# Kernel optimization log

Measured on AMD Instinct MI355X. Metric: run time of the kernel, lower is better.

Reference implementation:

```python
import jax, jax.numpy as jnp
import numpy as np

RADIUS = 0.2
NSAMPLE = 32
BANDWIDTH = 0.1


def ellipsoid_query(xyz, new_xyz, radius, nsample):
    """xyz:(B,N,3), new_xyz:(B,P,3) -> idx:(B,P,nsample) int32.
    Ellipsoid semi-axes (radius, 2*radius, radius); first nsample hits,
    padded with the first hit (index 0 if empty), matching the CUDA kernel.
    """
    B, N, _ = xyz.shape
    inv_sq = jnp.asarray([1.0 / radius**2, 1.0 / (2.0 * radius) ** 2, 1.0 / radius**2],
                         dtype=xyz.dtype)
    # accumulate per-coordinate to avoid a (B,P,N,3) intermediate
    q = jnp.zeros((B, new_xyz.shape[1], N), dtype=xyz.dtype)
    for k in range(3):
        d = new_xyz[:, :, None, k] - xyz[:, None, :, k]  # (B,P,N)
        q = q + d * d * inv_sq[k]
    mask = q < 1.0
    cand = jnp.where(mask, jnp.arange(N, dtype=jnp.int32), jnp.int32(N))  # invalid -> N
    cand = jnp.sort(cand, axis=-1)[..., :nsample]                          # (B,P,S)
    first = cand[..., :1]
    first = jnp.where(first >= N, jnp.int32(0), first)
    return jnp.where(cand >= N, first, cand)


def group(features, idx):
    """features:(B,C,N), idx:(B,P,S) -> (B,C,P,S)"""
    return jnp.take_along_axis(features[:, :, None, :], idx[:, None, :, :], axis=-1)


def setup_inputs() -> dict:
    key = jax.random.key(0)
    k1, k2, k3 = jax.random.split(key, 3)
    xyz = jax.random.uniform(k1, (4, 8192, 3), dtype=jnp.float32)
    new_xyz = jax.random.uniform(k2, (4, 2048, 3), dtype=jnp.float32)
    features = jax.random.normal(k3, (4, 64, 8192), dtype=jnp.float32)
    return {"xyz": xyz, "new_xyz": new_xyz, "features": features}


def reference(xyz, new_xyz, features):
    idx = ellipsoid_query(xyz, new_xyz, RADIUS, NSAMPLE)          # (B,P,S)
    xyz_trans = jnp.transpose(xyz, (0, 2, 1))                      # (B,3,N)
    grouped_xyz = group(xyz_trans, idx)                            # (B,3,P,S)
    # density: gaussian of distance to center
    g = jnp.transpose(grouped_xyz, (0, 2, 3, 1))                   # (B,P,S,3)
    dist = jnp.linalg.norm(g - new_xyz[:, :, None, :], axis=-1)    # (B,P,S)
    density = jnp.exp(-dist**2 / (2.0 * BANDWIDTH**2)) / (2.5 * BANDWIDTH)
    grouped_density = (1.0 / density)[:, None, :, :]               # (B,1,P,S)
    grouped_features = group(features, idx)                        # (B,C,P,S)
    return jnp.concatenate([grouped_xyz, grouped_density, grouped_features], axis=1)
```

## Files before the change

kernel.cpp:

```cpp
#include <hip/hip_runtime.h>

constexpr int NPTS = 8192;
constexpr int NQ   = 2048;
constexpr int NC   = 64;
constexpr int NS   = 32;
constexpr int NCH  = 3 + 1 + NC;
constexpr int CS   = NQ * NS;
constexpr int TP   = 2048;
constexpr int QPB  = 8;



union KLds {
    struct {
        float pts[3][TP + 1];
        int   idx[QPB][NS];
        int   ndone;
    } s;
    float tile[NC][65];
};

__device__ __forceinline__ unsigned prefix_popc(unsigned long long m) {
    return __builtin_amdgcn_mbcnt_hi((unsigned)(m >> 32),
           __builtin_amdgcn_mbcnt_lo((unsigned)m, 0u));
}

__global__ __launch_bounds__(512, 8) void scan_trans_kernel(
    const float* __restrict__ xyz,
    const float* __restrict__ nxyz,
    const float* __restrict__ feat,
    float* __restrict__ ftr,
    int* __restrict__ gidx,
    float* __restrict__ out,
    int ntrans)
{
    __shared__ KLds u;
    const int bx = blockIdx.x;
    const int t  = threadIdx.x;

    if (bx < ntrans) {
        const int b  = bx >> 7;
        const int tl = bx & 127;
        const int n0 = tl * 64;
        const float* fb = feat + (size_t)b * NC * NPTS;
        const int pl = t & 63;
        const int c0 = t >> 6;
        #pragma unroll
        for (int i = 0; i < 8; ++i) {
            const int c = c0 + 8 * i;
            u.tile[c][pl] = fb[(size_t)c * NPTS + n0 + pl];
        }
        __syncthreads();
        float* tb = ftr + ((size_t)b * NPTS + n0) * NC;
        #pragma unroll
        for (int i = 0; i < 8; ++i) {
            const int pp = c0 + 8 * i;
            tb[(size_t)pp * NC + pl] = u.tile[pl][pp];
        }
        return;
    }

    const int sb   = bx - ntrans;
    const int qpb  = NQ / QPB;
    const int b    = sb / qpb;
    const int p0   = (sb - b * qpb) * QPB;
    const int lane = t & 63;
    const int wave = t >> 6;
    const int p    = p0 + wave;
    const float* xb = xyz + (size_t)b * NPTS * 3;
    int* idx_row = u.s.idx[wave];

    const float qx = nxyz[((size_t)b * NQ + p) * 3 + 0];
    const float qy = nxyz[((size_t)b * NQ + p) * 3 + 1];
    const float qz = nxyz[((size_t)b * NQ + p) * 3 + 2];

    int cnt = 0;
    int first = -1;
    if (t == 0) u.s.ndone = 0;

    for (int tb = 0; tb < NPTS / TP; ++tb) {
        const float* src = xb + (size_t)tb * TP * 3;
        #pragma unroll
        for (int k = 0; k < 3 * TP / 512; ++k) {
            const int g  = k * 512 + t;
            const float val = src[g];
            const int pt = g / 3;
            const int c  = g - 3 * pt;
            u.s.pts[c][pt] = val;
        }
        __syncthreads();

        if (cnt < NS) {
            const int boff = tb * TP;
            for (int base = 0; base < TP; base += 128) {
                const int i0 = base + lane;
                const int i1 = i0 + 64;
                const float xA = u.s.pts[0][i0], xB = u.s.pts[0][i1];
                const float yA = u.s.pts[1][i0], yB = u.s.pts[1][i1];
                const float zA = u.s.pts[2][i0], zB = u.s.pts[2][i1];

                const float dxA = __fsub_rn(qx, xA);
                const float dyA = __fsub_rn(qy, yA);
                const float dzA = __fsub_rn(qz, zA);
                const float qA  = __fadd_rn(__fadd_rn(
                                    __fmul_rn(__fmul_rn(dxA, dxA), 25.0f),
                                    __fmul_rn(__fmul_rn(dyA, dyA), 6.25f)),
                                    __fmul_rn(__fmul_rn(dzA, dzA), 25.0f));
                const float dxB = __fsub_rn(qx, xB);
                const float dyB = __fsub_rn(qy, yB);
                const float dzB = __fsub_rn(qz, zB);
                const float qB  = __fadd_rn(__fadd_rn(
                                    __fmul_rn(__fmul_rn(dxB, dxB), 25.0f),
                                    __fmul_rn(__fmul_rn(dyB, dyB), 6.25f)),
                                    __fmul_rn(__fmul_rn(dzB, dzB), 25.0f));
                const bool hitA = qA < 1.0f;
                const bool hitB = qB < 1.0f;

                const unsigned long long m0 = __ballot(hitA);
                const unsigned long long m1 = __ballot(hitB);
                if (first < 0) {
                    if (m0 != 0ull)      first = boff + base + __builtin_ctzll(m0);
                    else if (m1 != 0ull) first = boff + base + 64 + __builtin_ctzll(m1);
                }
                if (hitA) {
                    const int pos = cnt + (int)prefix_popc(m0);
                    if (pos < NS) idx_row[pos] = boff + i0;
                }
                const int c0h = __popcll(m0);
                if (hitB) {
                    const int pos = cnt + c0h + (int)prefix_popc(m1);
                    if (pos < NS) idx_row[pos] = boff + i1;
                }
                cnt += c0h + __popcll(m1);
                if (cnt >= NS) break;
            }
            if (cnt >= NS && lane == 0)
                atomicAdd(&u.s.ndone, 1);
        }
        __syncthreads();
        if (u.s.ndone == QPB) break;
    }

    if (cnt < NS) {
        const int f = (cnt == 0) ? 0 : first;
        if (lane < NS && lane >= cnt) idx_row[lane] = f;
    }

    if (lane < NS) {
        const int s = lane;
        const int j = idx_row[s];
        gidx[((size_t)b * NQ + p) * NS + s] = j;

        const float px = xb[3 * j + 0];
        const float py = xb[3 * j + 1];
        const float pz = xb[3 * j + 2];
        const float dx = __fsub_rn(px, qx);
        const float dy = __fsub_rn(py, qy);
        const float dz = __fsub_rn(pz, qz);
        const float d2 = __fadd_rn(__fadd_rn(__fmul_rn(dx, dx), __fmul_rn(dy, dy)),
                                   __fmul_rn(dz, dz));
        const float dist = __fsqrt_rn(d2);
        const float arg  = __fdiv_rn(-__fmul_rn(dist, dist), 0.02f);
        const float density = __fmul_rn(expf(arg), 4.0f);
        const float gd = __fdiv_rn(1.0f, density);

        float* ob = out + ((size_t)b * NCH * NQ + p) * NS + s;
        ob[0 * (size_t)CS] = px;
        ob[1 * (size_t)CS] = py;
        ob[2 * (size_t)CS] = pz;
        ob[3 * (size_t)CS] = gd;
    }
}

__global__ __launch_bounds__(512, 8) void group_kernel(
    const int* __restrict__ gidx,
    const float* __restrict__ ftr,
    float* __restrict__ out,
    int B)
{
    __shared__ float ldsc[NC][33];

    const int g = blockIdx.x;
    int b, p;
    if (B == 4) {
        b = (g & 7) >> 1;
        p = ((g >> 3) << 1) | (g & 1);
    } else {
        b = g / NQ;
        p = g - b * NQ;
    }
    const int tid = threadIdx.x;

    const int cg = tid & 15;
    const int sl = tid >> 4;
    const int j  = gidx[((size_t)b * NQ + p) * NS + sl];
    const float4 v = ((const float4*)(ftr + ((size_t)b * NPTS + j) * NC))[cg];
    ldsc[4 * cg + 0][sl] = v.x;
    ldsc[4 * cg + 1][sl] = v.y;
    ldsc[4 * cg + 2][sl] = v.z;
    ldsc[4 * cg + 3][sl] = v.w;
    __syncthreads();

    const int c  = tid >> 3;
    const int s4 = (tid & 7) << 2;
    float4 w;
    w.x = ldsc[c][s4 + 0];
    w.y = ldsc[c][s4 + 1];
    w.z = ldsc[c][s4 + 2];
    w.w = ldsc[c][s4 + 3];
    float* op = out + (((size_t)b * NCH + 4 + c) * NQ + p) * NS + s4;
    *(float4*)op = w;
}

__global__ __launch_bounds__(512, 8) void ellip_direct_kernel(
    const float* __restrict__ xyz,
    const float* __restrict__ nxyz,
    const float* __restrict__ feat,
    float* __restrict__ out)
{
    __shared__ int idx_s[8][NS];

    const int b    = blockIdx.y;
    const int p0   = blockIdx.x * 8;
    const int tid  = threadIdx.x;
    const int lane = tid & 63;
    const int wave = tid >> 6;
    const float* xb = xyz + (size_t)b * NPTS * 3;

    {
        const int p = p0 + wave;
        const float qx = nxyz[((size_t)b * NQ + p) * 3 + 0];
        const float qy = nxyz[((size_t)b * NQ + p) * 3 + 1];
        const float qz = nxyz[((size_t)b * NQ + p) * 3 + 2];
        int cnt = 0, first = -1;
        for (int base = 0; base < NPTS; base += 64) {
            const int i = base + lane;
            const float dx = __fsub_rn(qx, xb[i * 3 + 0]);
            const float dy = __fsub_rn(qy, xb[i * 3 + 1]);
            const float dz = __fsub_rn(qz, xb[i * 3 + 2]);
            const float t0 = __fmul_rn(__fmul_rn(dx, dx), 25.0f);
            const float t1 = __fmul_rn(__fmul_rn(dy, dy), 6.25f);
            const float t2 = __fmul_rn(__fmul_rn(dz, dz), 25.0f);
            const float qv = __fadd_rn(__fadd_rn(t0, t1), t2);
            const bool hit = qv < 1.0f;
            const unsigned long long m = __ballot(hit);
            if (first < 0 && m != 0ull) first = base + __builtin_ctzll(m);
            if (hit) {
                const int pos = cnt + __popcll(m & ((1ull << lane) - 1ull));
                if (pos < NS) idx_s[wave][pos] = i;
            }
            cnt += __popcll(m);
            if (cnt >= NS) break;
        }
        if (cnt < NS) {
            const int f = (cnt == 0) ? 0 : first;
            if (lane < NS && lane >= cnt) idx_s[wave][lane] = f;
        }
    }
    __syncthreads();

    const int s = tid & 31;
    const int h = (tid >> 5) & 1;
    const int q = tid >> 6;
    const int p = p0 + q;
    const int j = idx_s[q][s];
    float* ob = out + ((size_t)b * NCH * NQ + p) * NS + s;

    if (h == 0) {
        const float qx = nxyz[((size_t)b * NQ + p) * 3 + 0];
        const float qy = nxyz[((size_t)b * NQ + p) * 3 + 1];
        const float qz = nxyz[((size_t)b * NQ + p) * 3 + 2];
        const float px = xb[j * 3 + 0], py = xb[j * 3 + 1], pz = xb[j * 3 + 2];
        const float dx = __fsub_rn(px, qx);
        const float dy = __fsub_rn(py, qy);
        const float dz = __fsub_rn(pz, qz);
        const float d2 = __fadd_rn(__fadd_rn(__fmul_rn(dx, dx), __fmul_rn(dy, dy)),
                                   __fmul_rn(dz, dz));
        const float dist = __fsqrt_rn(d2);
        const float arg  = __fdiv_rn(-__fmul_rn(dist, dist), 0.02f);
        const float gd = __fdiv_rn(1.0f, __fmul_rn(expf(arg), 4.0f));
        ob[0 * (size_t)CS] = px;
        ob[1 * (size_t)CS] = py;
        ob[2 * (size_t)CS] = pz;
        ob[3 * (size_t)CS] = gd;
    }
    const float* fb = feat + (size_t)b * NC * NPTS + j;
    #pragma unroll 4
    for (int c = h; c < NC; c += 2)
        ob[(size_t)(4 + c) * CS] = fb[(size_t)c * NPTS];
}

extern "C" void kernel_launch(void* const* d_in, const int* in_sizes, int n_in,
                              void* d_out, int out_size, void* d_ws, size_t ws_size,
                              hipStream_t stream) {
    const float* xyz  = (const float*)d_in[0];
    const float* nxyz = (const float*)d_in[1];
    const float* feat = (const float*)d_in[2];
    float* out = (float*)d_out;

    const int B = in_sizes[0] / (NPTS * 3);
    const size_t ftr_f = (size_t)B * NPTS * NC;
    const size_t idx_f = (size_t)B * NQ * NS;
    const size_t need  = (ftr_f + idx_f) * 4;

    if (ws_size >= need) {
        float* ftr = (float*)d_ws;
        int*   idx = (int*)(ftr + ftr_f);

        const int ntrans = B * (NPTS / 64);
        const int nscan  = B * (NQ / QPB);
        scan_trans_kernel<<<dim3(ntrans + nscan), 512, 0, stream>>>(
            xyz, nxyz, feat, ftr, idx, out, ntrans);
        group_kernel<<<dim3(B * NQ), 512, 0, stream>>>(idx, ftr, out, B);
    } else {
        ellip_direct_kernel<<<dim3(NQ / 8, B), 512, 0, stream>>>(xyz, nxyz, feat, out);
    }
}
```

Measured before the change: 101.0 us.

## Scan points directly from global memory per wave with register prefetch

Replaces the block-wide LDS staging of 2048-point tiles, and the __syncthreads/atomic termination vote, with each wave reading float3 points straight from global memory (L1/L2 cached) and double-buffering the next 128 points in registers. Each wave can now stop as soon as its own query has 32 hits instead of waiting for the whole block, and the LDS footprint shrinks, which may allow more blocks to be resident. The cost is redundant global/L2 reads across the eight waves in a block and unaligned 12-byte loads.

```diff
diff --git a/kernel.cpp b/kernel.cpp
--- a/kernel.cpp
+++ b/kernel.cpp
@@ -6,17 +6,12 @@
 constexpr int NS   = 32;
 constexpr int NCH  = 3 + 1 + NC;
 constexpr int CS   = NQ * NS;
-constexpr int TP   = 2048;
 constexpr int QPB  = 8;
 
 
 
 union KLds {
-    struct {
-        float pts[3][TP + 1];
-        int   idx[QPB][NS];
-        int   ndone;
-    } s;
+    int   idx[QPB][NS];
     float tile[NC][65];
 };
 
@@ -68,7 +63,8 @@
     const int wave = t >> 6;
     const int p    = p0 + wave;
     const float* xb = xyz + (size_t)b * NPTS * 3;
-    int* idx_row = u.s.idx[wave];
+    const float3* xb3 = reinterpret_cast<const float3*>(xb);
+    int* idx_row = u.idx[wave];
 
     const float qx = nxyz[((size_t)b * NQ + p) * 3 + 0];
     const float qy = nxyz[((size_t)b * NQ + p) * 3 + 1];
@@ -76,69 +72,53 @@
 
     int cnt = 0;
     int first = -1;
-    if (t == 0) u.s.ndone = 0;
-
-    for (int tb = 0; tb < NPTS / TP; ++tb) {
-        const float* src = xb + (size_t)tb * TP * 3;
-        #pragma unroll
-        for (int k = 0; k < 3 * TP / 512; ++k) {
-            const int g  = k * 512 + t;
-            const float val = src[g];
-            const int pt = g / 3;
-            const int c  = g - 3 * pt;
-            u.s.pts[c][pt] = val;
-        }
-        __syncthreads();
-
-        if (cnt < NS) {
-            const int boff = tb * TP;
-            for (int base = 0; base < TP; base += 128) {
-                const int i0 = base + lane;
-                const int i1 = i0 + 64;
-                const float xA = u.s.pts[0][i0], xB = u.s.pts[0][i1];
-                const float yA = u.s.pts[1][i0], yB = u.s.pts[1][i1];
-                const float zA = u.s.pts[2][i0], zB = u.s.pts[2][i1];
-
-                const float dxA = __fsub_rn(qx, xA);
-                const float dyA = __fsub_rn(qy, yA);
-                const float dzA = __fsub_rn(qz, zA);
-                const float qA  = __fadd_rn(__fadd_rn(
-                                    __fmul_rn(__fmul_rn(dxA, dxA), 25.0f),
-                                    __fmul_rn(__fmul_rn(dyA, dyA), 6.25f)),
-                                    __fmul_rn(__fmul_rn(dzA, dzA), 25.0f));
-                const float dxB = __fsub_rn(qx, xB);
-                const float dyB = __fsub_rn(qy, yB);
-                const float dzB = __fsub_rn(qz, zB);
-                const float qB  = __fadd_rn(__fadd_rn(
-                                    __fmul_rn(__fmul_rn(dxB, dxB), 25.0f),
-                                    __fmul_rn(__fmul_rn(dyB, dyB), 6.25f)),
-                                    __fmul_rn(__fmul_rn(dzB, dzB), 25.0f));
-                const bool hitA = qA < 1.0f;
-                const bool hitB = qB < 1.0f;
-
-                const unsigned long long m0 = __ballot(hitA);
-                const unsigned long long m1 = __ballot(hitB);
-                if (first < 0) {
-                    if (m0 != 0ull)      first = boff + base + __builtin_ctzll(m0);
-                    else if (m1 != 0ull) first = boff + base + 64 + __builtin_ctzll(m1);
-                }
-                if (hitA) {
-                    const int pos = cnt + (int)prefix_popc(m0);
-                    if (pos < NS) idx_row[pos] = boff + i0;
-                }
-                const int c0h = __popcll(m0);
-                if (hitB) {
-                    const int pos = cnt + c0h + (int)prefix_popc(m1);
-                    if (pos < NS) idx_row[pos] = boff + i1;
-                }
-                cnt += c0h + __popcll(m1);
-                if (cnt >= NS) break;
-            }
-            if (cnt >= NS && lane == 0)
-                atomicAdd(&u.s.ndone, 1);
-        }
-        __syncthreads();
-        if (u.s.ndone == QPB) break;
+
+    float3 A0 = xb3[lane];
+    float3 A1 = xb3[lane + 64];
+    for (int base = 0;;) {
+        const int nb = base + 128;
+        const int pf = nb & (NPTS - 1);
+        const float3 B0 = xb3[pf + lane];
+        const float3 B1 = xb3[pf + lane + 64];
+
+        const float dxA = __fsub_rn(qx, A0.x);
+        const float dyA = __fsub_rn(qy, A0.y);
+        const float dzA = __fsub_rn(qz, A0.z);
+        const float qA  = __fadd_rn(__fadd_rn(
+                            __fmul_rn(__fmul_rn(dxA, dxA), 25.0f),
+                            __fmul_rn(__fmul_rn(dyA, dyA), 6.25f)),
+                            __fmul_rn(__fmul_rn(dzA, dzA), 25.0f));
+        const float dxB = __fsub_rn(qx, A1.x);
+        const float dyB = __fsub_rn(qy, A1.y);
+        const float dzB = __fsub_rn(qz, A1.z);
+        const float qB  = __fadd_rn(__fadd_rn(
+                            __fmul_rn(__fmul_rn(dxB, dxB), 25.0f),
+                            __fmul_rn(__fmul_rn(dyB, dyB), 6.25f)),
+                            __fmul_rn(__fmul_rn(dzB, dzB), 25.0f));
+        const bool hitA = qA < 1.0f;
+        const bool hitB = qB < 1.0f;
+
+        const unsigned long long m0 = __ballot(hitA);
+        const unsigned long long m1 = __ballot(hitB);
+        if (first < 0) {
+            if (m0 != 0ull)      first = base + __builtin_ctzll(m0);
+            else if (m1 != 0ull) first = base + 64 + __builtin_ctzll(m1);
+        }
+        if (hitA) {
+            const int pos = cnt + (int)prefix_popc(m0);
+            if (pos < NS) idx_row[pos] = base + lane;
+        }
+        const int c0h = __popcll(m0);
+        if (hitB) {
+            const int pos = cnt + c0h + (int)prefix_popc(m1);
+            if (pos < NS) idx_row[pos] = base + 64 + lane;
+        }
+        cnt += c0h + __popcll(m1);
+
+        base = nb;
+        if (cnt >= NS || base >= NPTS) break;
+        A0 = B0;
+        A1 = B1;
     }
 
     if (cnt < NS) {
```

New measurement: 101.2 us. No clear change (+0.2%).
